# Performance work log

Measured on AMD Instinct MI355X. Metric: run time of the kernel, lower is better.

Reference implementation:

```python
import jax, jax.numpy as jnp
import numpy as np

D_MODEL, D_STATE, D_CONV, EXPAND, MLP_EXPAND = 1024, 16, 4, 2, 2
D_INNER = EXPAND * D_MODEL          # 2048
DT_RANK = D_MODEL // 16             # 64
B, L = 2, 1024


def setup_inputs() -> dict:
    key = jax.random.key(0)
    ks = jax.random.split(key, 16)
    s = 0.02
    inp = {
        "x": jax.random.normal(ks[0], (B, L, D_MODEL), jnp.float32),
        "ln1_w": jnp.ones((D_MODEL,), jnp.float32),
        "ln1_b": jnp.zeros((D_MODEL,), jnp.float32),
        "in_proj_w": jax.random.normal(ks[1], (2 * D_INNER, D_MODEL), jnp.float32) * s,
        "conv_w": jax.random.normal(ks[2], (D_INNER, 1, D_CONV), jnp.float32) * s,
        "conv_b": jnp.zeros((D_INNER,), jnp.float32),
        "x_proj_w": jax.random.normal(ks[3], (DT_RANK + 2 * D_STATE, D_INNER), jnp.float32) * s,
        "dt_proj_w": jax.random.normal(ks[4], (D_INNER, DT_RANK), jnp.float32) * s,
        "dt_proj_b": jax.random.uniform(ks[5], (D_INNER,), jnp.float32, -4.0, -2.0),
        "A_log": jnp.tile(jnp.log(jnp.arange(1, D_STATE + 1, dtype=jnp.float32))[None, :], (D_INNER, 1)),
        "D": jnp.ones((D_INNER,), jnp.float32),
        "out_proj_w": jax.random.normal(ks[6], (D_MODEL, D_INNER), jnp.float32) * s,
        "ln2_w": jnp.ones((D_MODEL,), jnp.float32),
        "ln2_b": jnp.zeros((D_MODEL,), jnp.float32),
        "mlp_w1": jax.random.normal(ks[7], (MLP_EXPAND * D_MODEL, D_MODEL), jnp.float32) * s,
        "mlp_b1": jnp.zeros((MLP_EXPAND * D_MODEL,), jnp.float32),
        "mlp_w2": jax.random.normal(ks[8], (D_MODEL, MLP_EXPAND * D_MODEL), jnp.float32) * s,
        "mlp_b2": jnp.zeros((D_MODEL,), jnp.float32),
    }
    return inp


def _layernorm(x, w, b, eps=1e-5):
    mu = jnp.mean(x, -1, keepdims=True)
    var = jnp.var(x, -1, keepdims=True)
    return (x - mu) * jax.lax.rsqrt(var + eps) * w + b


def _mamba(x, in_proj_w, conv_w, conv_b, x_proj_w, dt_proj_w, dt_proj_b, A_log, D, out_proj_w):
    # x: (B, L, d_model)
    xz = jnp.einsum('bld,ed->ble', x, in_proj_w)          # (B, L, 2*d_inner)
    u, z = jnp.split(xz, 2, axis=-1)                      # each (B, L, d_inner)
    # depthwise causal conv over time
    u_c = jnp.transpose(u, (0, 2, 1))                     # (B, d_inner, L)
    u_c = jax.lax.conv_general_dilated(
        u_c, conv_w, window_strides=(1,), padding=[(D_CONV - 1, 0)],
        dimension_numbers=('NCH', 'OIH', 'NCH'), feature_group_count=D_INNER)
    u = jax.nn.silu(jnp.transpose(u_c, (0, 2, 1)) + conv_b)  # (B, L, d_inner)

    dbc = jnp.einsum('bld,ed->ble', u, x_proj_w)          # (B, L, dt_rank+2*d_state)
    dt, Bm, Cm = jnp.split(dbc, [DT_RANK, DT_RANK + D_STATE], axis=-1)
    delta = jax.nn.softplus(jnp.einsum('blr,dr->bld', dt, dt_proj_w) + dt_proj_b)  # (B, L, d_inner)

    A = -jnp.exp(A_log)                                   # (d_inner, d_state)
    deltaA = jnp.exp(delta[..., None] * A)                # (B, L, d_inner, d_state)
    deltaBu = delta[..., None] * Bm[:, :, None, :] * u[..., None]

    def step(h, inp):
        dA, dBu, Ct = inp
        h = dA * h + dBu                                  # (B, d_inner, d_state)
        y = jnp.einsum('bdn,bn->bd', h, Ct)
        return h, y

    h0 = jnp.zeros((x.shape[0], D_INNER, D_STATE), x.dtype)
    xs = (jnp.moveaxis(deltaA, 1, 0), jnp.moveaxis(deltaBu, 1, 0), jnp.moveaxis(Cm, 1, 0))
    _, ys = jax.lax.scan(step, h0, xs)                    # (L, B, d_inner)
    y = jnp.moveaxis(ys, 0, 1) + u * D                    # (B, L, d_inner)
    y = y * jax.nn.silu(z)
    return jnp.einsum('ble,de->bld', y, out_proj_w)


def reference(x, ln1_w, ln1_b, in_proj_w, conv_w, conv_b, x_proj_w, dt_proj_w, dt_proj_b,
              A_log, D, out_proj_w, ln2_w, ln2_b, mlp_w1, mlp_b1, mlp_w2, mlp_b2):
    h = x + _mamba(_layernorm(x, ln1_w, ln1_b), in_proj_w, conv_w, conv_b,
                   x_proj_w, dt_proj_w, dt_proj_b, A_log, D, out_proj_w)
    y = _layernorm(h, ln2_w, ln2_b)
    y = jax.nn.gelu(jnp.einsum('bld,ed->ble', y, mlp_w1) + mlp_b1, approximate=False)
    y = jnp.einsum('ble,de->bld', y, mlp_w2) + mlp_b2
    return h + y
```

## Files before the change

kernel.cpp:

```cpp
#include <hip/hip_runtime.h>
#include <hip/hip_bf16.h>
#include <math.h>

typedef __hip_bfloat16 bf16;
typedef __attribute__((ext_vector_type(8))) short bf16x8;
typedef __attribute__((ext_vector_type(4))) float f32x4;

__device__ __forceinline__ float b2f(bf16 x) { return __bfloat162float(x); }
__device__ __forceinline__ float us2f(unsigned short u) {
    return __uint_as_float(((unsigned int)u) << 16);
}
__device__ __forceinline__ unsigned short f2us(float f) {
    bf16 t = __float2bfloat16(f);
    return *reinterpret_cast<unsigned short*>(&t);
}
__device__ __forceinline__ float scrub(float v) {
    return (v == v && fabsf(v) < 3.0e38f) ? v : 0.f;
}
__device__ __forceinline__ float to_float(float x) { return x; }
__device__ __forceinline__ float to_float(bf16 x) { return __bfloat162float(x); }
__device__ __forceinline__ void store_out(float* p, float v) { *p = v; }
__device__ __forceinline__ void store_out(bf16* p, float v) { *p = __float2bfloat16(v); }

__device__ __forceinline__ void cp16(const void* g, void* l) {
    __builtin_amdgcn_global_load_lds(
        (const __attribute__((address_space(1))) unsigned int*)g,
        (__attribute__((address_space(3))) unsigned int*)l, 16, 0, 0);
}

struct Ptrs { const void* p[18]; };

__constant__ __device__ const long TOFF[19] = {
    0,         2097152,  2098176,  2099200,  6293504,  6301696,  6303744,
    6500352,   6631424,  6633472,  6666240,  6668288,  8765440,  8766464,
    8767488,   10864640, 10866688, 12963840, 12964864};

__global__ __launch_bounds__(256) void convert_ln1_kernel(
    Ptrs ptrs, unsigned short* __restrict__ dst, bf16* __restrict__ out)
{
    __shared__ float red[8];
    if (blockIdx.x < 5307) {
        const long g = 262144 + (long)blockIdx.x * 256 + threadIdx.x;
        if (g >= 1620608) return;
        const long e0 = g * 8;
        int t = 1;
        #pragma unroll
        for (int i = 2; i < 18; ++i) t += (e0 >= TOFF[i]) ? 1 : 0;
        const long local = e0 - TOFF[t];
        const float4* ps = (const float4*)((const float*)ptrs.p[t] + local);
        const float4 a = ps[0], b = ps[1];
        ushort4 o0, o1;
        o0.x = f2us(a.x); o0.y = f2us(a.y); o0.z = f2us(a.z); o0.w = f2us(a.w);
        o1.x = f2us(b.x); o1.y = f2us(b.y); o1.z = f2us(b.z); o1.w = f2us(b.w);
        *(ushort4*)(dst + e0)     = o0;
        *(ushort4*)(dst + e0 + 4) = o1;
        return;
    }
    const int row = blockIdx.x - 5307;
    const int tid = threadIdx.x;
    const float* xf = (const float*)ptrs.p[0];
    const float4 raw = ((const float4*)(xf + (long)row * 1024))[tid];
    float v[4] = {raw.x, raw.y, raw.z, raw.w};
    float s  = v[0] + v[1] + v[2] + v[3];
    float s2 = v[0]*v[0] + v[1]*v[1] + v[2]*v[2] + v[3]*v[3];
    #pragma unroll
    for (int o = 32; o > 0; o >>= 1) {
        s  += __shfl_xor(s, o);
        s2 += __shfl_xor(s2, o);
    }
    if ((tid & 63) == 0) { red[tid >> 6] = s; red[4 + (tid >> 6)] = s2; }
    __syncthreads();
    s  = red[0] + red[1] + red[2] + red[3];
    s2 = red[4] + red[5] + red[6] + red[7];
    const float mu  = s * (1.f / 1024.f);
    const float var = fmaxf(s2 * (1.f / 1024.f) - mu * mu, 0.f);
    const float rs  = rsqrtf(var + 1e-5f);
    const float4 w4 = ((const float4*)ptrs.p[1])[tid];
    const float4 b4 = ((const float4*)ptrs.p[2])[tid];
    ushort4 o;
    o.x = f2us((v[0] - mu) * rs * w4.x + b4.x);
    o.y = f2us((v[1] - mu) * rs * w4.y + b4.y);
    o.z = f2us((v[2] - mu) * rs * w4.z + b4.z);
    o.w = f2us((v[3] - mu) * rs * w4.w + b4.w);
    ((ushort4*)((unsigned short*)out + (long)row * 1024))[tid] = o;
}

template <typename TIN>
__global__ __launch_bounds__(256) void ln_kernel(
    const TIN* __restrict__ in, const bf16* __restrict__ gw,
    const bf16* __restrict__ gb, bf16* __restrict__ out)
{
    const int row = blockIdx.x;
    const int tid = threadIdx.x;
    float v[4];
    if constexpr (sizeof(TIN) == 2) {
        ushort4 raw = ((const ushort4*)((const unsigned short*)in + (long)row * 1024))[tid];
        v[0] = us2f(raw.x); v[1] = us2f(raw.y); v[2] = us2f(raw.z); v[3] = us2f(raw.w);
    } else {
        float4 raw = ((const float4*)((const float*)in + (long)row * 1024))[tid];
        v[0] = raw.x; v[1] = raw.y; v[2] = raw.z; v[3] = raw.w;
    }
    float s  = v[0] + v[1] + v[2] + v[3];
    float s2 = v[0]*v[0] + v[1]*v[1] + v[2]*v[2] + v[3]*v[3];
    #pragma unroll
    for (int o = 32; o > 0; o >>= 1) {
        s  += __shfl_xor(s, o);
        s2 += __shfl_xor(s2, o);
    }
    __shared__ float red[8];
    if ((tid & 63) == 0) { red[tid >> 6] = s; red[4 + (tid >> 6)] = s2; }
    __syncthreads();
    s  = red[0] + red[1] + red[2] + red[3];
    s2 = red[4] + red[5] + red[6] + red[7];
    const float mu  = s * (1.f / 1024.f);
    const float var = fmaxf(s2 * (1.f / 1024.f) - mu * mu, 0.f);
    const float rs  = rsqrtf(var + 1e-5f);
    const int c0 = tid * 4;
    ushort4 o;
    o.x = f2us((v[0] - mu) * rs * b2f(gw[c0 + 0]) + b2f(gb[c0 + 0]));
    o.y = f2us((v[1] - mu) * rs * b2f(gw[c0 + 1]) + b2f(gb[c0 + 1]));
    o.z = f2us((v[2] - mu) * rs * b2f(gw[c0 + 2]) + b2f(gb[c0 + 2]));
    o.w = f2us((v[3] - mu) * rs * b2f(gw[c0 + 3]) + b2f(gb[c0 + 3]));
    ((ushort4*)((unsigned short*)out + (long)row * 1024))[tid] = o;
}

template <int BM, int BN, int ACT, bool NG, typename TOUT, typename TRES>
__global__ __launch_bounds__(256) void gemm_as(
    const bf16* __restrict__ A, int lda,
    const bf16* __restrict__ Bw, int ldb,
    TOUT* __restrict__ C, int ldc,
    const bf16* __restrict__ bias,
    const TRES* __restrict__ res,
    int M, int N, int K)
{
    constexpr int AI = BM / 32;
    constexpr int BJ = BN / 32;
    __shared__ __align__(16) short As[BM * 64];
    __shared__ __align__(16) short Bs[BN * 64];
    const int tid  = threadIdx.x;
    const int lane = tid & 63;
    const int wv   = tid >> 6;
    const int m0 = blockIdx.y * BM;
    const int n0 = blockIdx.x * BN;
    const int wm = (wv >> 1) * (BM / 2);
    const int wn = (wv & 1) * (BN / 2);
    const int lr = lane & 15;
    const int lq = lane >> 4;
    const int grow = lane >> 3;
    const int gcol = (lane & 7) * 8;

    if (NG) {
        const int z0 = (N - n0) * 64;
        uint4 z; z.x = z.y = z.z = z.w = 0;
        for (int s = z0 + tid * 8; s < BN * 64; s += 2048)
            *(uint4*)&Bs[s] = z;
    }

    f32x4 acc[AI][BJ] = {};

    for (int k0 = 0; k0 < K; k0 += 64) {
        #pragma unroll
        for (int g = 0; g < BM / 32; ++g) {
            const int gg = g * 4 + wv;
            cp16(A + (long)(m0 + gg * 8 + grow) * lda + k0 + gcol, &As[gg * 512]);
        }
        #pragma unroll
        for (int g = 0; g < BN / 32; ++g) {
            const int gg = g * 4 + wv;
            if (!NG || n0 + gg * 8 < N)
                cp16(Bw + (long)(n0 + gg * 8 + grow) * ldb + k0 + gcol, &Bs[gg * 512]);
        }
        __syncthreads();

        #pragma unroll
        for (int kk = 0; kk < 2; ++kk) {
            bf16x8 af[AI], bfr[BJ];
            #pragma unroll
            for (int i = 0; i < AI; ++i)
                af[i] = *(const bf16x8*)&As[(wm + i * 16 + lr) * 64 + kk * 32 + lq * 8];
            #pragma unroll
            for (int j = 0; j < BJ; ++j)
                bfr[j] = *(const bf16x8*)&Bs[(wn + j * 16 + lr) * 64 + kk * 32 + lq * 8];
            #pragma unroll
            for (int i = 0; i < AI; ++i)
                #pragma unroll
                for (int j = 0; j < BJ; ++j)
                    acc[i][j] = __builtin_amdgcn_mfma_f32_16x16x32_bf16(
                        af[i], bfr[j], acc[i][j], 0, 0, 0);
        }
        __syncthreads();
    }

    #pragma unroll
    for (int j = 0; j < BJ; ++j) {
        const int col = n0 + wn + j * 16 + lr;
        if (col >= N) continue;
        const float bv = bias ? b2f(bias[col]) : 0.f;
        #pragma unroll
        for (int i = 0; i < AI; ++i) {
            const int r0 = m0 + wm + i * 16 + lq * 4;
            #pragma unroll
            for (int r = 0; r < 4; ++r) {
                const long row = r0 + r;
                float v = acc[i][j][r] + bv;
                if (ACT == 1) v = 0.5f * v * (1.f + erff(v * 0.70710678118f));
                if (ACT == 2) v = (v > 20.f) ? v : __logf(1.f + __expf(v));
                if (res) v += to_float(res[row * (long)ldc + col]);
                store_out(&C[row * (long)ldc + col], scrub(v));
            }
        }
    }
}

__global__ __launch_bounds__(256) void gemm_xproj_sk(
    const bf16* __restrict__ A,
    const bf16* __restrict__ Bw,
    float* __restrict__ P)
{
    constexpr int N = 96;
    __shared__ __align__(16) short As[64 * 64];
    __shared__ __align__(16) short Bs[64 * 64];
    const int tid  = threadIdx.x;
    const int lane = tid & 63;
    const int wv   = tid >> 6;
    const int m0 = blockIdx.y * 64;
    const int n0 = blockIdx.x * 64;
    const int kz = blockIdx.z;
    const int wm = (wv >> 1) * 32;
    const int wn = (wv & 1) * 32;
    const int lr = lane & 15;
    const int lq = lane >> 4;
    const int grow = lane >> 3;
    const int gcol = (lane & 7) * 8;

    {
        const int z0 = (N - n0) * 64;
        uint4 z; z.x = z.y = z.z = z.w = 0;
        for (int s = z0 + tid * 8; s < 64 * 64; s += 2048)
            *(uint4*)&Bs[s] = z;
    }

    f32x4 acc[2][2] = {};
    const int kend = kz * 512 + 512;
    for (int k0 = kz * 512; k0 < kend; k0 += 64) {
        #pragma unroll
        for (int g = 0; g < 2; ++g) {
            const int gg = g * 4 + wv;
            cp16(A + (long)(m0 + gg * 8 + grow) * 2048 + k0 + gcol, &As[gg * 512]);
        }
        #pragma unroll
        for (int g = 0; g < 2; ++g) {
            const int gg = g * 4 + wv;
            if (n0 + gg * 8 < N)
                cp16(Bw + (long)(n0 + gg * 8 + grow) * 2048 + k0 + gcol, &Bs[gg * 512]);
        }
        __syncthreads();
        #pragma unroll
        for (int kk = 0; kk < 2; ++kk) {
            bf16x8 af[2], bfr[2];
            #pragma unroll
            for (int i = 0; i < 2; ++i)
                af[i] = *(const bf16x8*)&As[(wm + i * 16 + lr) * 64 + kk * 32 + lq * 8];
            #pragma unroll
            for (int j = 0; j < 2; ++j)
                bfr[j] = *(const bf16x8*)&Bs[(wn + j * 16 + lr) * 64 + kk * 32 + lq * 8];
            #pragma unroll
            for (int i = 0; i < 2; ++i)
                #pragma unroll
                for (int j = 0; j < 2; ++j)
                    acc[i][j] = __builtin_amdgcn_mfma_f32_16x16x32_bf16(
                        af[i], bfr[j], acc[i][j], 0, 0, 0);
        }
        __syncthreads();
    }

    float* Pz = P + (long)kz * (2048 * 96);
    #pragma unroll
    for (int j = 0; j < 2; ++j) {
        const int col = n0 + wn + j * 16 + lr;
        if (col >= N) continue;
        #pragma unroll
        for (int i = 0; i < 2; ++i) {
            const int r0 = m0 + wm + i * 16 + lq * 4;
            #pragma unroll
            for (int r = 0; r < 4; ++r)
                Pz[(long)(r0 + r) * 96 + col] = acc[i][j][r];
        }
    }
}

__global__ __launch_bounds__(256) void xproj_reduce(
    const float* __restrict__ P, bf16* __restrict__ dbc)
{
    const int i = blockIdx.x * 256 + threadIdx.x;
    const float s = P[i] + P[i + 196608] + P[i + 2 * 196608] + P[i + 3 * 196608];
    dbc[i] = __float2bfloat16(scrub(s));
}

__global__ __launch_bounds__(256) void conv_silu_kernel(
    const bf16* __restrict__ xz, const bf16* __restrict__ cw,
    const bf16* __restrict__ cb, bf16* __restrict__ uc)
{
    const int gid = blockIdx.x * 256 + threadIdx.x;
    const int dc  = (gid & 255) * 8;
    const int row = gid >> 8;
    const int t   = row & 1023;
    const bf16x8 w0 = *(const bf16x8*)(cw + dc * 4);
    const bf16x8 w1 = *(const bf16x8*)(cw + dc * 4 + 8);
    const bf16x8 w2 = *(const bf16x8*)(cw + dc * 4 + 16);
    const bf16x8 w3 = *(const bf16x8*)(cw + dc * 4 + 24);
    const bf16x8 bv = *(const bf16x8*)(cb + dc);
    float wf[32];
    #pragma unroll
    for (int k = 0; k < 8; ++k) {
        wf[k]      = us2f((unsigned short)w0[k]);
        wf[8 + k]  = us2f((unsigned short)w1[k]);
        wf[16 + k] = us2f((unsigned short)w2[k]);
        wf[24 + k] = us2f((unsigned short)w3[k]);
    }
    float acc[8];
    #pragma unroll
    for (int i = 0; i < 8; ++i) acc[i] = us2f((unsigned short)bv[i]);
    #pragma unroll
    for (int j = 0; j < 4; ++j) {
        const int tt = t - 3 + j;
        if (tt < 0) continue;
        const bf16x8 xv = *(const bf16x8*)(xz + (long)(row - 3 + j) * 4096 + dc);
        #pragma unroll
        for (int i = 0; i < 8; ++i)
            acc[i] += wf[i * 4 + j] * us2f((unsigned short)xv[i]);
    }
    bf16x8 o;
    #pragma unroll
    for (int i = 0; i < 8; ++i) {
        const float sg = 1.f / (1.f + __expf(-acc[i]));
        o[i] = (short)f2us(acc[i] * sg);
    }
    *(bf16x8*)(uc + (long)row * 2048 + dc) = o;
}

__global__ __launch_bounds__(256) void scan_kernel(
    const bf16* __restrict__ delta,
    const bf16* __restrict__ uc,
    const bf16* __restrict__ dbc,
    const bf16* __restrict__ xz,
    const float* __restrict__ A_log,
    const float* __restrict__ Dp,
    bf16* __restrict__ y)
{
    const int b   = blockIdx.y;
    const int d0  = blockIdx.x * 16;
    const int tid = threadIdx.x;
    const int n   = tid & 15;
    const int dl  = tid >> 4;
    const int d   = d0 + dl;

    __shared__ __align__(16) float2 sDU[64][17];
    __shared__ __align__(16) float2 sBC[64][17];
    __shared__ __align__(16) float  sZ [64][17];
    __shared__ __align__(16) float  sP [64][16][20];

    const float An = -expf(A_log[d * 16 + n]);
    const float Dd = Dp[d];
    float h = 0.f;
    const long rowbase = (long)b * 1024;

    const int dl3 = tid & 15;
    const int t3  = tid >> 4;

    const int ltt = tid >> 2;
    const int ldg = (tid & 3) * 4;

    ushort4 rDT, rUV, rB, rC, rZ;
    auto load_chunk = [&](int t0c) {
        const long r = rowbase + t0c + ltt;
        rDT = *(const ushort4*)((const unsigned short*)delta + r * 2048 + d0 + ldg);
        rUV = *(const ushort4*)((const unsigned short*)uc    + r * 2048 + d0 + ldg);
        rB  = *(const ushort4*)((const unsigned short*)dbc   + r * 96 + 64 + ldg);
        rC  = *(const ushort4*)((const unsigned short*)dbc   + r * 96 + 80 + ldg);
        rZ  = *(const ushort4*)((const unsigned short*)xz    + r * 4096 + 2048 + d0 + ldg);
    };
    auto store_chunk = [&]() {
        const unsigned short dt4[4] = {rDT.x, rDT.y, rDT.z, rDT.w};
        const unsigned short uv4[4] = {rUV.x, rUV.y, rUV.z, rUV.w};
        const unsigned short b4_[4] = {rB.x,  rB.y,  rB.z,  rB.w};
        const unsigned short c4_[4] = {rC.x,  rC.y,  rC.z,  rC.w};
        const unsigned short z4_[4] = {rZ.x,  rZ.y,  rZ.z,  rZ.w};
        #pragma unroll
        for (int j = 0; j < 4; ++j) {
            sDU[ltt][ldg + j] = float2{us2f(dt4[j]), us2f(uv4[j])};
            sBC[ltt][ldg + j] = float2{us2f(b4_[j]), us2f(c4_[j])};
            const float zz = us2f(z4_[j]);
            sZ[ltt][ldg + j] = zz / (1.f + __expf(-zz));
        }
    };

    load_chunk(0);
    for (int t0 = 0; t0 < 1024; t0 += 64) {
        store_chunk();
        __syncthreads();
        if (t0 + 64 < 1024) load_chunk(t0 + 64);

        {
            float2 dua[8], bca[8], dub[8], bcb[8];
            #pragma unroll
            for (int t = 0; t < 8; ++t) { dua[t] = sDU[t][dl]; bca[t] = sBC[t][n]; }
            #pragma unroll
            for (int tb = 0; tb < 64; tb += 8) {
                if (tb < 56) {
                    #pragma unroll
                    for (int t = 0; t < 8; ++t) {
                        dub[t] = sDU[tb + 8 + t][dl];
                        bcb[t] = sBC[tb + 8 + t][n];
                    }
                }
                #pragma unroll
                for (int t = 0; t < 8; ++t) {
                    const float a = __expf(dua[t].x * An);
                    h = a * h + (dua[t].x * dua[t].y) * bca[t].x;
                    float p = h * bca[t].y;
                    if (n == 0) p += dua[t].y * Dd;
                    sP[tb + t][dl][n] = p;
                }
                #pragma unroll
                for (int t = 0; t < 8; ++t) { dua[t] = dub[t]; bca[t] = bcb[t]; }
            }
        }
        __syncthreads();

        #pragma unroll
        for (int k = 0; k < 4; ++k) {
            const int t = t3 + k * 16;
            const float4* pp = (const float4*)&sP[t][dl3][0];
            const float4 p0 = pp[0], p1 = pp[1], p2 = pp[2], p3 = pp[3];
            const float s = ((p0.x + p0.y) + (p0.z + p0.w))
                          + ((p1.x + p1.y) + (p1.z + p1.w))
                          + ((p2.x + p2.y) + (p2.z + p2.w))
                          + ((p3.x + p3.y) + (p3.z + p3.w));
            const float yv = s * sZ[t][dl3];
            y[(rowbase + t0 + t) * 2048 + d0 + dl3] = __float2bfloat16(yv);
        }
        __syncthreads();
    }
}

extern "C" void kernel_launch(void* const* d_in, const int* in_sizes, int n_in,
                              void* d_out, int out_size, void* d_ws, size_t ws_size,
                              hipStream_t stream)
{
    char* ws = (char*)d_ws;
    const size_t MiB = 1048576;

    bf16*  xn  = (bf16*)(ws);
    bf16*  xz  = (bf16*)(ws +  4 * MiB);
    bf16*  uc  = (bf16*)(ws + 20 * MiB);
    bf16*  dbc = (bf16*)(ws + 28 * MiB);
    bf16*  dlb = (bf16*)(ws + 28 * MiB + 524288);
    bf16*  yb  = dlb;
    float* hb  = (float*)(ws);
    float* xpp = (float*)(ws);
    bf16*  hn  = (bf16*)(ws +  8 * MiB);
    bf16*  gb  = (bf16*)(ws + 12 * MiB);
    unsigned short* cvt = (unsigned short*)(ws + 37 * MiB);

    const float* xf     = (const float*)d_in[0];
    const float* A_logf = (const float*)d_in[9];
    const float* Dpf    = (const float*)d_in[10];

    const bf16* in_proj_w  = (const bf16*)(cvt + 2099200);
    const bf16* conv_w     = (const bf16*)(cvt + 6293504);
    const bf16* conv_b     = (const bf16*)(cvt + 6301696);
    const bf16* x_proj_w   = (const bf16*)(cvt + 6303744);
    const bf16* dt_proj_w  = (const bf16*)(cvt + 6500352);
    const bf16* dt_proj_b  = (const bf16*)(cvt + 6631424);
    const bf16* out_proj_w = (const bf16*)(cvt + 6668288);
    const bf16* ln2_w      = (const bf16*)(cvt + 8765440);
    const bf16* ln2_b      = (const bf16*)(cvt + 8766464);
    const bf16* mlp_w1     = (const bf16*)(cvt + 8767488);
    const bf16* mlp_b1     = (const bf16*)(cvt + 10864640);
    const bf16* mlp_w2     = (const bf16*)(cvt + 10866688);
    const bf16* mlp_b2     = (const bf16*)(cvt + 12963840);

    Ptrs ptrs;
    for (int i = 0; i < 18; ++i) ptrs.p[i] = d_in[i];
    convert_ln1_kernel<<<7355, 256, 0, stream>>>(ptrs, cvt, xn);

    gemm_as<128, 128, 0, false, bf16, bf16><<<dim3(32, 16), 256, 0, stream>>>(
        xn, 1024, in_proj_w, 1024, xz, 4096, nullptr, (const bf16*)nullptr, 2048, 4096, 1024);
    conv_silu_kernel<<<2048, 256, 0, stream>>>(xz, conv_w, conv_b, uc);
    gemm_xproj_sk<<<dim3(2, 32, 4), 256, 0, stream>>>(uc, x_proj_w, xpp);
    xproj_reduce<<<768, 256, 0, stream>>>(xpp, dbc);
    gemm_as<64, 64, 2, false, bf16, bf16><<<dim3(32, 32), 256, 0, stream>>>(
        dbc, 96, dt_proj_w, 64, dlb, 2048, dt_proj_b, (const bf16*)nullptr, 2048, 2048, 64);
    scan_kernel<<<dim3(128, 2), 256, 0, stream>>>(dlb, uc, dbc, xz, A_logf, Dpf, yb);
    gemm_as<64, 64, 0, false, float, float><<<dim3(16, 32), 256, 0, stream>>>(
        yb, 2048, out_proj_w, 2048, hb, 1024, nullptr, xf, 2048, 1024, 2048);
    ln_kernel<float><<<2048, 256, 0, stream>>>(hb, ln2_w, ln2_b, hn);
    gemm_as<128, 64, 1, false, bf16, bf16><<<dim3(32, 16), 256, 0, stream>>>(
        hn, 1024, mlp_w1, 1024, gb, 2048, mlp_b1, (const bf16*)nullptr, 2048, 2048, 1024);
    gemm_as<64, 64, 0, false, float, float><<<dim3(16, 32), 256, 0, stream>>>(
        gb, 2048, mlp_w2, 2048, (float*)d_out, 1024, mlp_b2, hb, 2048, 1024, 2048);
}
```

Measured before the change: 326.1 us.

## Split selective scan into chunked carry, combine, and apply passes

Replaces the single sequential scan over 1024 timesteps (256 blocks) with a three-phase chunked scan. The first pass computes per-chunk decay products and end states over 8 chunks of 128 steps, a small kernel propagates the carries across chunks, and the apply pass rescans each chunk from its carried state. This gives 8x more blocks to fill the GPU and shortens the serial dependency chain, at the cost of recomputing the recurrence twice and adding two launches. It also replaces the shared-memory reduction over the state dimension with DPP row-shift adds, which removes the sP buffer and one barrier per chunk.

```diff
diff --git a/kernel.cpp b/kernel.cpp
--- a/kernel.cpp
+++ b/kernel.cpp
@@ -21,6 +21,13 @@
 __device__ __forceinline__ float to_float(bf16 x) { return __bfloat162float(x); }
 __device__ __forceinline__ void store_out(float* p, float v) { *p = v; }
 __device__ __forceinline__ void store_out(bf16* p, float v) { *p = __float2bfloat16(v); }
+
+template <int CTRL>
+__device__ __forceinline__ float dpp_shr_add(float x) {
+    const int sh = __builtin_amdgcn_update_dpp(
+        0, __float_as_int(x), CTRL, 0xF, 0xF, true);
+    return x + __int_as_float(sh);
+}
 
 __device__ __forceinline__ void cp16(const void* g, void* l) {
     __builtin_amdgcn_global_load_lds(
@@ -339,16 +346,109 @@
     *(bf16x8*)(uc + (long)row * 2048 + dc) = o;
 }
 
-__global__ __launch_bounds__(256) void scan_kernel(
+__global__ __launch_bounds__(256) void scan_carry_kernel(
+    const bf16* __restrict__ delta,
+    const bf16* __restrict__ uc,
+    const bf16* __restrict__ dbc,
+    const float* __restrict__ A_log,
+    float2* __restrict__ carry)
+{
+    const int b   = blockIdx.y;
+    const int c   = blockIdx.z;
+    const int d0  = blockIdx.x * 16;
+    const int tid = threadIdx.x;
+    const int n   = tid & 15;
+    const int dl  = tid >> 4;
+    const int d   = d0 + dl;
+
+    __shared__ __align__(16) float2 sDU[64][17];
+    __shared__ __align__(16) float  sB [64][17];
+
+    const float An = -expf(A_log[d * 16 + n]);
+    float h = 0.f, prod = 1.f;
+    const long rowbase = (long)b * 1024 + c * 128;
+
+    const int ltt = tid >> 2;
+    const int ldg = (tid & 3) * 4;
+
+    ushort4 rDT, rUV, rB;
+    auto load_chunk = [&](int t0c) {
+        const long r = rowbase + t0c + ltt;
+        rDT = *(const ushort4*)((const unsigned short*)delta + r * 2048 + d0 + ldg);
+        rUV = *(const ushort4*)((const unsigned short*)uc    + r * 2048 + d0 + ldg);
+        rB  = *(const ushort4*)((const unsigned short*)dbc   + r * 96 + 64 + ldg);
+    };
+    auto store_chunk = [&]() {
+        const unsigned short dt4[4] = {rDT.x, rDT.y, rDT.z, rDT.w};
+        const unsigned short uv4[4] = {rUV.x, rUV.y, rUV.z, rUV.w};
+        const unsigned short b4_[4] = {rB.x,  rB.y,  rB.z,  rB.w};
+        #pragma unroll
+        for (int j = 0; j < 4; ++j) {
+            sDU[ltt][ldg + j] = float2{us2f(dt4[j]), us2f(uv4[j])};
+            sB [ltt][ldg + j] = us2f(b4_[j]);
+        }
+    };
+
+    load_chunk(0);
+    for (int t0 = 0; t0 < 128; t0 += 64) {
+        store_chunk();
+        __syncthreads();
+        if (t0 + 64 < 128) load_chunk(t0 + 64);
+
+        float2 dua[8], dub[8];
+        float  ba[8], bb[8];
+        #pragma unroll
+        for (int t = 0; t < 8; ++t) { dua[t] = sDU[t][dl]; ba[t] = sB[t][n]; }
+        #pragma unroll
+        for (int tb = 0; tb < 64; tb += 8) {
+            if (tb < 56) {
+                #pragma unroll
+                for (int t = 0; t < 8; ++t) {
+                    dub[t] = sDU[tb + 8 + t][dl];
+                    bb[t]  = sB [tb + 8 + t][n];
+                }
+            }
+            #pragma unroll
+            for (int t = 0; t < 8; ++t) {
+                const float a = __expf(dua[t].x * An);
+                h = a * h + (dua[t].x * dua[t].y) * ba[t];
+                prod *= a;
+            }
+            #pragma unroll
+            for (int t = 0; t < 8; ++t) { dua[t] = dub[t]; ba[t] = bb[t]; }
+        }
+        __syncthreads();
+    }
+    carry[((long)b * 8 + c) * 32768 + d * 16 + n] = float2{prod, h};
+}
+
+__global__ __launch_bounds__(256) void scan_combine_kernel(float2* __restrict__ carry)
+{
+    const int gid = blockIdx.x * 256 + threadIdx.x;
+    const int b   = gid >> 15;
+    const int rem = gid & 32767;
+    float h = 0.f;
+    #pragma unroll
+    for (int c = 0; c < 8; ++c) {
+        float2* p = &carry[((long)b * 8 + c) * 32768 + rem];
+        const float2 AB = *p;
+        ((float*)p)[0] = h;
+        h = AB.x * h + AB.y;
+    }
+}
+
+__global__ __launch_bounds__(256) void scan_apply_kernel(
     const bf16* __restrict__ delta,
     const bf16* __restrict__ uc,
     const bf16* __restrict__ dbc,
     const bf16* __restrict__ xz,
     const float* __restrict__ A_log,
     const float* __restrict__ Dp,
+    const float2* __restrict__ carry,
     bf16* __restrict__ y)
 {
     const int b   = blockIdx.y;
+    const int c   = blockIdx.z;
     const int d0  = blockIdx.x * 16;
     const int tid = threadIdx.x;
     const int n   = tid & 15;
@@ -358,15 +458,11 @@
     __shared__ __align__(16) float2 sDU[64][17];
     __shared__ __align__(16) float2 sBC[64][17];
     __shared__ __align__(16) float  sZ [64][17];
-    __shared__ __align__(16) float  sP [64][16][20];
 
     const float An = -expf(A_log[d * 16 + n]);
     const float Dd = Dp[d];
-    float h = 0.f;
-    const long rowbase = (long)b * 1024;
-
-    const int dl3 = tid & 15;
-    const int t3  = tid >> 4;
+    float h = carry[((long)b * 8 + c) * 32768 + d * 16 + n].x;
+    const long rowbase = (long)b * 1024 + c * 128;
 
     const int ltt = tid >> 2;
     const int ldg = (tid & 3) * 4;
@@ -396,49 +492,40 @@
     };
 
     load_chunk(0);
-    for (int t0 = 0; t0 < 1024; t0 += 64) {
+    for (int t0 = 0; t0 < 128; t0 += 64) {
         store_chunk();
         __syncthreads();
-        if (t0 + 64 < 1024) load_chunk(t0 + 64);
-
-        {
-            float2 dua[8], bca[8], dub[8], bcb[8];
-            #pragma unroll
-            for (int t = 0; t < 8; ++t) { dua[t] = sDU[t][dl]; bca[t] = sBC[t][n]; }
-            #pragma unroll
-            for (int tb = 0; tb < 64; tb += 8) {
-                if (tb < 56) {
-                    #pragma unroll
-                    for (int t = 0; t < 8; ++t) {
-                        dub[t] = sDU[tb + 8 + t][dl];
-                        bcb[t] = sBC[tb + 8 + t][n];
-                    }
-                }
+        if (t0 + 64 < 128) load_chunk(t0 + 64);
+
+        float2 dua[8], bca[8], dub[8], bcb[8];
+        #pragma unroll
+        for (int t = 0; t < 8; ++t) { dua[t] = sDU[t][dl]; bca[t] = sBC[t][n]; }
+        #pragma unroll
+        for (int tb = 0; tb < 64; tb += 8) {
+            if (tb < 56) {
                 #pragma unroll
                 for (int t = 0; t < 8; ++t) {
-                    const float a = __expf(dua[t].x * An);
-                    h = a * h + (dua[t].x * dua[t].y) * bca[t].x;
-                    float p = h * bca[t].y;
-                    if (n == 0) p += dua[t].y * Dd;
-                    sP[tb + t][dl][n] = p;
+                    dub[t] = sDU[tb + 8 + t][dl];
+                    bcb[t] = sBC[tb + 8 + t][n];
                 }
-                #pragma unroll
-                for (int t = 0; t < 8; ++t) { dua[t] = dub[t]; bca[t] = bcb[t]; }
             }
-        }
-        __syncthreads();
-
-        #pragma unroll
-        for (int k = 0; k < 4; ++k) {
-            const int t = t3 + k * 16;
-            const float4* pp = (const float4*)&sP[t][dl3][0];
-            const float4 p0 = pp[0], p1 = pp[1], p2 = pp[2], p3 = pp[3];
-            const float s = ((p0.x + p0.y) + (p0.z + p0.w))
-                          + ((p1.x + p1.y) + (p1.z + p1.w))
-                          + ((p2.x + p2.y) + (p2.z + p2.w))
-                          + ((p3.x + p3.y) + (p3.z + p3.w));
-            const float yv = s * sZ[t][dl3];
-            y[(rowbase + t0 + t) * 2048 + d0 + dl3] = __float2bfloat16(yv);
+            #pragma unroll
+            for (int t = 0; t < 8; ++t) {
+                const float a = __expf(dua[t].x * An);
+                h = a * h + (dua[t].x * dua[t].y) * bca[t].x;
+                float p = h * bca[t].y;
+                if (n == 0) p += dua[t].y * Dd;
+                p = dpp_shr_add<0x111>(p);
+                p = dpp_shr_add<0x112>(p);
+                p = dpp_shr_add<0x114>(p);
+                p = dpp_shr_add<0x118>(p);
+                if (n == 15) {
+                    const float yv = p * sZ[tb + t][dl];
+                    y[(rowbase + t0 + tb + t) * 2048 + d] = __float2bfloat16(yv);
+                }
+            }
+            #pragma unroll
+            for (int t = 0; t < 8; ++t) { dua[t] = dub[t]; bca[t] = bcb[t]; }
         }
         __syncthreads();
     }
@@ -459,6 +546,7 @@
     bf16*  yb  = dlb;
     float* hb  = (float*)(ws);
     float* xpp = (float*)(ws);
+    float2* carry = (float2*)(ws);
     bf16*  hn  = (bf16*)(ws +  8 * MiB);
     bf16*  gb  = (bf16*)(ws + 12 * MiB);
     unsigned short* cvt = (unsigned short*)(ws + 37 * MiB);
@@ -492,7 +580,10 @@
     xproj_reduce<<<768, 256, 0, stream>>>(xpp, dbc);
     gemm_as<64, 64, 2, false, bf16, bf16><<<dim3(32, 32), 256, 0, stream>>>(
         dbc, 96, dt_proj_w, 64, dlb, 2048, dt_proj_b, (const bf16*)nullptr, 2048, 2048, 64);
-    scan_kernel<<<dim3(128, 2), 256, 0, stream>>>(dlb, uc, dbc, xz, A_logf, Dpf, yb);
+    scan_carry_kernel<<<dim3(128, 2, 8), 256, 0, stream>>>(dlb, uc, dbc, A_logf, carry);
+    scan_combine_kernel<<<256, 256, 0, stream>>>(carry);
+    scan_apply_kernel<<<dim3(128, 2, 8), 256, 0, stream>>>(
+        dlb, uc, dbc, xz, A_logf, Dpf, carry, yb);
     gemm_as<64, 64, 0, false, float, float><<<dim3(16, 32), 256, 0, stream>>>(
         yb, 2048, out_proj_w, 2048, hb, 1024, nullptr, xf, 2048, 1024, 2048);
     ln_kernel<float><<<2048, 256, 0, stream>>>(hb, ln2_w, ln2_b, hn);
```

Result: slower. 371.2 us (+13.8%).

## Replace sequential selective scan with chunked three-pass parallel scan

Applied to the files above, without the earlier changes.

The single-pass scan, which ran only 256 blocks walking all 1024 timesteps, is split into three kernels. The first computes a per-chunk decay product and local state for 16 chunks of 64 steps. The second combines these carries sequentially across chunks. The third reruns each chunk from its carried-in state and emits the gated output. Each thread now holds all 16 states of one channel in registers, which removes the shared-memory reduction across states and gives 16x more blocks along time. The cost is reading delta, u and B twice, two extra launches, and borrowing the output buffer as carry scratch.

```diff
diff --git a/kernel.cpp b/kernel.cpp
--- a/kernel.cpp
+++ b/kernel.cpp
@@ -339,108 +339,219 @@
     *(bf16x8*)(uc + (long)row * 2048 + dc) = o;
 }
 
-__global__ __launch_bounds__(256) void scan_kernel(
+__global__ __launch_bounds__(128) void scan_carry_kernel(
+    const bf16* __restrict__ delta,
+    const bf16* __restrict__ uc,
+    const bf16* __restrict__ dbc,
+    const float* __restrict__ A_log,
+    float2* __restrict__ carry)
+{
+    const int d0  = blockIdx.x * 128;
+    const int b   = blockIdx.y;
+    const int c   = blockIdx.z;
+    const int tid = threadIdx.x;
+    const int lane = tid & 63;
+    const int wv   = tid >> 6;
+    const int d    = d0 + tid;
+
+    __shared__ __align__(16) unsigned short sDT[64][128];
+    __shared__ __align__(16) unsigned short sU [64][128];
+    __shared__ __align__(16) float sB[64][16];
+
+    float An[16];
+    {
+        const float4* ap = (const float4*)(A_log + (long)d * 16);
+        #pragma unroll
+        for (int q = 0; q < 4; ++q) {
+            const float4 a4 = ap[q];
+            An[q*4+0] = -expf(a4.x); An[q*4+1] = -expf(a4.y);
+            An[q*4+2] = -expf(a4.z); An[q*4+3] = -expf(a4.w);
+        }
+    }
+
+    const long r0 = (long)b * 1024 + c * 64;
+
+    const int srow = lane >> 4;
+    const int scol = (lane & 15) * 8;
+    #pragma unroll
+    for (int g = 0; g < 8; ++g) {
+        const int grp = g * 2 + wv;
+        const long r = r0 + grp * 4 + srow;
+        cp16((const unsigned short*)delta + r * 2048 + d0 + scol, &sDT[grp * 4][0]);
+        cp16((const unsigned short*)uc    + r * 2048 + d0 + scol, &sU [grp * 4][0]);
+    }
+    #pragma unroll
+    for (int k = 0; k < 2; ++k) {
+        const int q = tid + k * 128;
+        const int row = q >> 2, quad = q & 3;
+        const ushort4 v = *(const ushort4*)((const unsigned short*)dbc
+                              + (r0 + row) * 96 + 64 + quad * 4);
+        sB[row][quad*4+0] = us2f(v.x); sB[row][quad*4+1] = us2f(v.y);
+        sB[row][quad*4+2] = us2f(v.z); sB[row][quad*4+3] = us2f(v.w);
+    }
+
+    float h[16], pr[16];
+    #pragma unroll
+    for (int n = 0; n < 16; ++n) { h[n] = 0.f; pr[n] = 1.f; }
+    __syncthreads();
+
+    #pragma unroll 2
+    for (int t = 0; t < 64; ++t) {
+        const float dt = us2f(sDT[t][tid]);
+        const float u  = us2f(sU [t][tid]);
+        const float s  = dt * u;
+        const float4 b0 = *(const float4*)&sB[t][0];
+        const float4 b1 = *(const float4*)&sB[t][4];
+        const float4 b2 = *(const float4*)&sB[t][8];
+        const float4 b3 = *(const float4*)&sB[t][12];
+        const float Bv[16] = {b0.x,b0.y,b0.z,b0.w, b1.x,b1.y,b1.z,b1.w,
+                              b2.x,b2.y,b2.z,b2.w, b3.x,b3.y,b3.z,b3.w};
+        #pragma unroll
+        for (int n = 0; n < 16; ++n) {
+            const float a = __expf(dt * An[n]);
+            h[n]  = a * h[n] + s * Bv[n];
+            pr[n] *= a;
+        }
+    }
+    float2* cp = carry + ((long)(b * 16 + c) * 32768 + (long)d * 16);
+    #pragma unroll
+    for (int n = 0; n < 16; ++n) cp[n] = float2{pr[n], h[n]};
+}
+
+__global__ __launch_bounds__(256) void scan_combine_kernel(float2* __restrict__ carry)
+{
+    const int gid = blockIdx.x * 256 + threadIdx.x;
+    const int b   = gid >> 15;
+    const int rem = gid & 32767;
+    float h = 0.f;
+    #pragma unroll
+    for (int c = 0; c < 16; ++c) {
+        float2* p = &carry[((long)b * 16 + c) * 32768 + rem];
+        const float2 AB = *p;
+        ((float*)p)[0] = h;
+        h = AB.x * h + AB.y;
+    }
+}
+
+__global__ __launch_bounds__(128) void scan_apply_kernel(
     const bf16* __restrict__ delta,
     const bf16* __restrict__ uc,
     const bf16* __restrict__ dbc,
     const bf16* __restrict__ xz,
     const float* __restrict__ A_log,
     const float* __restrict__ Dp,
+    const float2* __restrict__ carry,
     bf16* __restrict__ y)
 {
+    const int d0  = blockIdx.x * 128;
     const int b   = blockIdx.y;
-    const int d0  = blockIdx.x * 16;
+    const int c   = blockIdx.z;
     const int tid = threadIdx.x;
-    const int n   = tid & 15;
-    const int dl  = tid >> 4;
-    const int d   = d0 + dl;
-
-    __shared__ __align__(16) float2 sDU[64][17];
-    __shared__ __align__(16) float2 sBC[64][17];
-    __shared__ __align__(16) float  sZ [64][17];
-    __shared__ __align__(16) float  sP [64][16][20];
-
-    const float An = -expf(A_log[d * 16 + n]);
+    const int lane = tid & 63;
+    const int wv   = tid >> 6;
+    const int d    = d0 + tid;
+
+    __shared__ __align__(16) unsigned short sDT[64][128];
+    __shared__ __align__(16) unsigned short sU [64][128];
+    __shared__ __align__(16) unsigned short sZ [64][128];
+    __shared__ __align__(16) float sB[64][16];
+    __shared__ __align__(16) float sC[64][16];
+
+    float An[16];
+    {
+        const float4* ap = (const float4*)(A_log + (long)d * 16);
+        #pragma unroll
+        for (int q = 0; q < 4; ++q) {
+            const float4 a4 = ap[q];
+            An[q*4+0] = -expf(a4.x); An[q*4+1] = -expf(a4.y);
+            An[q*4+2] = -expf(a4.z); An[q*4+3] = -expf(a4.w);
+        }
+    }
     const float Dd = Dp[d];
-    float h = 0.f;
-    const long rowbase = (long)b * 1024;
-
-    const int dl3 = tid & 15;
-    const int t3  = tid >> 4;
-
-    const int ltt = tid >> 2;
-    const int ldg = (tid & 3) * 4;
-
-    ushort4 rDT, rUV, rB, rC, rZ;
-    auto load_chunk = [&](int t0c) {
-        const long r = rowbase + t0c + ltt;
-        rDT = *(const ushort4*)((const unsigned short*)delta + r * 2048 + d0 + ldg);
-        rUV = *(const ushort4*)((const unsigned short*)uc    + r * 2048 + d0 + ldg);
-        rB  = *(const ushort4*)((const unsigned short*)dbc   + r * 96 + 64 + ldg);
-        rC  = *(const ushort4*)((const unsigned short*)dbc   + r * 96 + 80 + ldg);
-        rZ  = *(const ushort4*)((const unsigned short*)xz    + r * 4096 + 2048 + d0 + ldg);
-    };
-    auto store_chunk = [&]() {
-        const unsigned short dt4[4] = {rDT.x, rDT.y, rDT.z, rDT.w};
-        const unsigned short uv4[4] = {rUV.x, rUV.y, rUV.z, rUV.w};
-        const unsigned short b4_[4] = {rB.x,  rB.y,  rB.z,  rB.w};
-        const unsigned short c4_[4] = {rC.x,  rC.y,  rC.z,  rC.w};
-        const unsigned short z4_[4] = {rZ.x,  rZ.y,  rZ.z,  rZ.w};
-        #pragma unroll
-        for (int j = 0; j < 4; ++j) {
-            sDU[ltt][ldg + j] = float2{us2f(dt4[j]), us2f(uv4[j])};
-            sBC[ltt][ldg + j] = float2{us2f(b4_[j]), us2f(c4_[j])};
-            const float zz = us2f(z4_[j]);
-            sZ[ltt][ldg + j] = zz / (1.f + __expf(-zz));
-        }
-    };
-
-    load_chunk(0);
-    for (int t0 = 0; t0 < 1024; t0 += 64) {
-        store_chunk();
-        __syncthreads();
-        if (t0 + 64 < 1024) load_chunk(t0 + 64);
-
-        {
-            float2 dua[8], bca[8], dub[8], bcb[8];
-            #pragma unroll
-            for (int t = 0; t < 8; ++t) { dua[t] = sDU[t][dl]; bca[t] = sBC[t][n]; }
-            #pragma unroll
-            for (int tb = 0; tb < 64; tb += 8) {
-                if (tb < 56) {
-                    #pragma unroll
-                    for (int t = 0; t < 8; ++t) {
-                        dub[t] = sDU[tb + 8 + t][dl];
-                        bcb[t] = sBC[tb + 8 + t][n];
-                    }
-                }
-                #pragma unroll
-                for (int t = 0; t < 8; ++t) {
-                    const float a = __expf(dua[t].x * An);
-                    h = a * h + (dua[t].x * dua[t].y) * bca[t].x;
-                    float p = h * bca[t].y;
-                    if (n == 0) p += dua[t].y * Dd;
-                    sP[tb + t][dl][n] = p;
-                }
-                #pragma unroll
-                for (int t = 0; t < 8; ++t) { dua[t] = dub[t]; bca[t] = bcb[t]; }
-            }
-        }
-        __syncthreads();
-
-        #pragma unroll
-        for (int k = 0; k < 4; ++k) {
-            const int t = t3 + k * 16;
-            const float4* pp = (const float4*)&sP[t][dl3][0];
-            const float4 p0 = pp[0], p1 = pp[1], p2 = pp[2], p3 = pp[3];
-            const float s = ((p0.x + p0.y) + (p0.z + p0.w))
-                          + ((p1.x + p1.y) + (p1.z + p1.w))
-                          + ((p2.x + p2.y) + (p2.z + p2.w))
-                          + ((p3.x + p3.y) + (p3.z + p3.w));
-            const float yv = s * sZ[t][dl3];
-            y[(rowbase + t0 + t) * 2048 + d0 + dl3] = __float2bfloat16(yv);
-        }
-        __syncthreads();
+
+    const long r0 = (long)b * 1024 + c * 64;
+
+    const int srow = lane >> 4;
+    const int scol = (lane & 15) * 8;
+    #pragma unroll
+    for (int g = 0; g < 8; ++g) {
+        const int grp = g * 2 + wv;
+        const long r = r0 + grp * 4 + srow;
+        cp16((const unsigned short*)delta + r * 2048 + d0 + scol, &sDT[grp * 4][0]);
+        cp16((const unsigned short*)uc    + r * 2048 + d0 + scol, &sU [grp * 4][0]);
+        cp16((const unsigned short*)xz    + r * 4096 + 2048 + d0 + scol, &sZ[grp * 4][0]);
+    }
+    #pragma unroll
+    for (int k = 0; k < 4; ++k) {
+        const int q = tid + k * 128;
+        const int row = q >> 3, quad = q & 7;
+        const ushort4 v = *(const ushort4*)((const unsigned short*)dbc
+                              + (r0 + row) * 96 + 64 + quad * 4);
+        float* dst = (quad < 4) ? &sB[row][quad * 4] : &sC[row][(quad - 4) * 4];
+        dst[0] = us2f(v.x); dst[1] = us2f(v.y); dst[2] = us2f(v.z); dst[3] = us2f(v.w);
+    }
+
+    float h[16];
+    {
+        const float4* hp = (const float4*)(carry + ((long)(b * 16 + c) * 32768
+                                                    + (long)d * 16));
+        #pragma unroll
+        for (int k = 0; k < 8; ++k) {
+            const float4 v = hp[k];
+            h[2*k]   = v.x;
+            h[2*k+1] = v.z;
+        }
+    }
+    __syncthreads();
+
+    unsigned short* yp = (unsigned short*)y + r0 * 2048 + d;
+
+    #pragma unroll 2
+    for (int t = 0; t < 64; ++t) {
+        const float dt = us2f(sDT[t][tid]);
+        const float u  = us2f(sU [t][tid]);
+        const float zz = us2f(sZ [t][tid]);
+        const float s  = dt * u;
+        const float4 b0 = *(const float4*)&sB[t][0];
+        const float4 b1 = *(const float4*)&sB[t][4];
+        const float4 b2 = *(const float4*)&sB[t][8];
+        const float4 b3 = *(const float4*)&sB[t][12];
+        const float4 c0 = *(const float4*)&sC[t][0];
+        const float4 c1 = *(const float4*)&sC[t][4];
+        const float4 c2 = *(const float4*)&sC[t][8];
+        const float4 c3 = *(const float4*)&sC[t][12];
+        const float Bv[16] = {b0.x,b0.y,b0.z,b0.w, b1.x,b1.y,b1.z,b1.w,
+                              b2.x,b2.y,b2.z,b2.w, b3.x,b3.y,b3.z,b3.w};
+        const float Cv[16] = {c0.x,c0.y,c0.z,c0.w, c1.x,c1.y,c1.z,c1.w,
+                              c2.x,c2.y,c2.z,c2.w, c3.x,c3.y,c3.z,c3.w};
+        float y0 = 0.f, y1 = 0.f, y2 = 0.f, y3 = 0.f;
+        #pragma unroll
+        for (int n = 0; n < 4; ++n) {
+            const float a = __expf(dt * An[n]);
+            h[n] = a * h[n] + s * Bv[n];
+            y0 += h[n] * Cv[n];
+        }
+        #pragma unroll
+        for (int n = 4; n < 8; ++n) {
+            const float a = __expf(dt * An[n]);
+            h[n] = a * h[n] + s * Bv[n];
+            y1 += h[n] * Cv[n];
+        }
+        #pragma unroll
+        for (int n = 8; n < 12; ++n) {
+            const float a = __expf(dt * An[n]);
+            h[n] = a * h[n] + s * Bv[n];
+            y2 += h[n] * Cv[n];
+        }
+        #pragma unroll
+        for (int n = 12; n < 16; ++n) {
+            const float a = __expf(dt * An[n]);
+            h[n] = a * h[n] + s * Bv[n];
+            y3 += h[n] * Cv[n];
+        }
+        const float ys  = (y0 + y1) + (y2 + y3) + u * Dd;
+        const float sil = zz / (1.f + __expf(-zz));
+        yp[(long)t * 2048] = f2us(ys * sil);
     }
 }
 
@@ -459,6 +570,7 @@
     bf16*  yb  = dlb;
     float* hb  = (float*)(ws);
     float* xpp = (float*)(ws);
+    float2* carry = (float2*)d_out;
     bf16*  hn  = (bf16*)(ws +  8 * MiB);
     bf16*  gb  = (bf16*)(ws + 12 * MiB);
     unsigned short* cvt = (unsigned short*)(ws + 37 * MiB);
@@ -492,7 +604,10 @@
     xproj_reduce<<<768, 256, 0, stream>>>(xpp, dbc);
     gemm_as<64, 64, 2, false, bf16, bf16><<<dim3(32, 32), 256, 0, stream>>>(
         dbc, 96, dt_proj_w, 64, dlb, 2048, dt_proj_b, (const bf16*)nullptr, 2048, 2048, 64);
-    scan_kernel<<<dim3(128, 2), 256, 0, stream>>>(dlb, uc, dbc, xz, A_logf, Dpf, yb);
+    scan_carry_kernel<<<dim3(16, 2, 16), 128, 0, stream>>>(dlb, uc, dbc, A_logf, carry);
+    scan_combine_kernel<<<256, 256, 0, stream>>>(carry);
+    scan_apply_kernel<<<dim3(16, 2, 16), 128, 0, stream>>>(
+        dlb, uc, dbc, xz, A_logf, Dpf, carry, yb);
     gemm_as<64, 64, 0, false, float, float><<<dim3(16, 32), 256, 0, stream>>>(
         yb, 2048, out_proj_w, 2048, hb, 1024, nullptr, xf, 2048, 1024, 2048);
     ln_kernel<float><<<2048, 256, 0, stream>>>(hb, ln2_w, ln2_b, hn);
```

Result: no change. 327.3 us (+0.4%).
